# Kernel tuning notes

Hardware: AMD Instinct MI355X
Metric: run time of the kernel (lower is better)

Reference implementation:

```python
import jax, jax.numpy as jnp
import numpy as np

D = 256      # model dim
H = 8        # heads
DH = 32      # dim per head
M = 110      # nb random features = int(32*ln(32))
DEPTH = 6
DFF = 1024   # ff_mult * D


def _layer_norm(x, g, b):
    mu = jnp.mean(x, -1, keepdims=True)
    var = jnp.mean(jnp.square(x - mu), -1, keepdims=True)
    return (x - mu) * jax.lax.rsqrt(var + 1e-5) * g + b


def _softmax_kernel(x, proj, is_query):
    # FAVOR+ positive softmax kernel features (performer-pytorch softmax_kernel)
    dn = x.shape[-1] ** -0.25
    ratio = proj.shape[0] ** -0.5
    xd = jnp.einsum('bhnd,md->bhnm', x * dn, proj)
    diag = 0.5 * jnp.sum(jnp.square(x), -1, keepdims=True) * dn * dn
    stab = jnp.max(xd, -1, keepdims=True) if is_query else jnp.max(xd)
    return ratio * (jnp.exp(xd - diag - stab) + 1e-3)


def _linear_attention(q, k, v):
    # non-causal linear attention: O(N*m*d) instead of O(N^2)
    k_sum = jnp.sum(k, axis=2)                               # [B,H,m]
    d_inv = 1.0 / jnp.einsum('bhnm,bhm->bhn', q, k_sum)      # [B,H,N]
    ctx = jnp.einsum('bhnm,bhnd->bhmd', k, v)                # [B,H,m,dh]
    return jnp.einsum('bhnm,bhmd,bhn->bhnd', q, ctx, d_inv)


def _forward(expr, token_emb, cls_token, ln1_g, ln1_b, Wq, bq, Wk, bk, Wv, bv,
             Wo, bo, ln2_g, ln2_b, W1, b1, W2, b2, proj_mat, Wp, bp, top_k_genes):
    B = expr.shape[0]
    vals, _ = jax.lax.top_k(expr, top_k_genes)               # [B, k] sorted desc (matches torch.topk)
    # preprocess: L1 normalize (eps=1e-12 like F.normalize) -> *1e4 -> log1p -> 7 bins
    norm = vals / jnp.maximum(jnp.sum(jnp.abs(vals), -1, keepdims=True), 1e-12)
    e = jnp.log1p(norm * 10000.0)
    bins = jnp.linspace(0.0, jnp.max(e), 8)
    # torch.bucketize(right=False) == searchsorted side='left'
    tokens = jnp.clip(jnp.searchsorted(bins[:-1], e, side='left'), 0, 6)
    x = jnp.concatenate([jnp.broadcast_to(cls_token, (B, 1, D)), token_emb[tokens]], axis=1)
    N = x.shape[1]
    for i in range(DEPTH):
        # pre-norm FAVOR+ attention block
        h = _layer_norm(x, ln1_g[i], ln1_b[i])
        q = (h @ Wq[i] + bq[i]).reshape(B, N, H, DH).transpose(0, 2, 1, 3)
        k = (h @ Wk[i] + bk[i]).reshape(B, N, H, DH).transpose(0, 2, 1, 3)
        v = (h @ Wv[i] + bv[i]).reshape(B, N, H, DH).transpose(0, 2, 1, 3)
        qp = _softmax_kernel(q, proj_mat[i], True)
        kp = _softmax_kernel(k, proj_mat[i], False)
        o = _linear_attention(qp, kp, v).transpose(0, 2, 1, 3).reshape(B, N, D)
        x = x + o @ Wo[i] + bo[i]
        # pre-norm FFN block (GELU exact, like torch default)
        h2 = _layer_norm(x, ln2_g[i], ln2_b[i])
        x = x + jax.nn.gelu(h2 @ W1[i] + b1[i], approximate=False) @ W2[i] + b2[i]
    return x[:, 0] @ Wp + bp


def setup_inputs() -> dict:
    key = jax.random.key(0)
    ks = jax.random.split(key, 12)
    s = 0.02
    return {
        'expr': jax.random.uniform(ks[0], (8, 16906), dtype=jnp.float32),
        'token_emb': jax.random.normal(ks[1], (7, D), dtype=jnp.float32) * s,
        'cls_token': jax.random.normal(ks[2], (1, 1, D), dtype=jnp.float32),
        'ln1_g': jnp.ones((DEPTH, D), jnp.float32),
        'ln1_b': jnp.zeros((DEPTH, D), jnp.float32),
        'Wq': jax.random.normal(ks[3], (DEPTH, D, D), dtype=jnp.float32) * s,
        'bq': jnp.zeros((DEPTH, D), jnp.float32),
        'Wk': jax.random.normal(ks[4], (DEPTH, D, D), dtype=jnp.float32) * s,
        'bk': jnp.zeros((DEPTH, D), jnp.float32),
        'Wv': jax.random.normal(ks[5], (DEPTH, D, D), dtype=jnp.float32) * s,
        'bv': jnp.zeros((DEPTH, D), jnp.float32),
        'Wo': jax.random.normal(ks[6], (DEPTH, D, D), dtype=jnp.float32) * s,
        'bo': jnp.zeros((DEPTH, D), jnp.float32),
        'ln2_g': jnp.ones((DEPTH, D), jnp.float32),
        'ln2_b': jnp.zeros((DEPTH, D), jnp.float32),
        'W1': jax.random.normal(ks[7], (DEPTH, D, DFF), dtype=jnp.float32) * s,
        'b1': jnp.zeros((DEPTH, DFF), jnp.float32),
        'W2': jax.random.normal(ks[8], (DEPTH, DFF, D), dtype=jnp.float32) * s,
        'b2': jnp.zeros((DEPTH, D), jnp.float32),
        'proj_mat': jax.random.normal(ks[9], (DEPTH, M, DH), dtype=jnp.float32),
        'Wp': jax.random.normal(ks[10], (D, D), dtype=jnp.float32) * s,
        'bp': jnp.zeros((D,), jnp.float32),
        'top_k_genes': 2048,
    }


def reference(expr, token_emb, cls_token, ln1_g, ln1_b, Wq, bq, Wk, bk, Wv, bv,
              Wo, bo, ln2_g, ln2_b, W1, b1, W2, b2, proj_mat, Wp, bp, top_k_genes):
    return _forward(expr, token_emb, cls_token, ln1_g, ln1_b, Wq, bq, Wk, bk, Wv, bv,
                    Wo, bo, ln2_g, ln2_b, W1, b1, W2, b2, proj_mat, Wp, bp, top_k_genes)
```

## Files before the change

### kernel.cpp

```cpp
#include <hip/hip_runtime.h>
#include <hip/hip_bf16.h>

#define B_    8
#define NG    16906
#define KSEL  2048
#define D_    256
#define H_    8
#define DH    32
#define M_    110
#define DEPTH_ 6
#define DFF_  1024
#define N_    2049
#define BN_   (B_*N_)
#define QS    768
#define NC    8
#define NTILES 33
#define CTXE  (M_*33)
#define CTXN2 (64*CTXE)
#define NIT_TK 17

static constexpr float DN    = 0.42044820762685725f;
static constexpr float DN2   = 0.17677669529663687f;
static constexpr float RATIO = 0.09534625892455922f;

typedef __attribute__((ext_vector_type(8))) short s8v;
typedef __attribute__((ext_vector_type(4))) float f4v;

__device__ __forceinline__ unsigned floatToOrdered(float f){
  unsigned b = __float_as_uint(f);
  return (b & 0x80000000u) ? ~b : (b | 0x80000000u);
}
__device__ __forceinline__ float orderedToFloat(unsigned u){
  unsigned b = (u & 0x80000000u) ? (u & 0x7FFFFFFFu) : ~u;
  return __uint_as_float(b);
}
__device__ __forceinline__ unsigned short f2us(float f){
  __hip_bfloat16 b = __float2bfloat16(f);
  return *reinterpret_cast<unsigned short*>(&b);
}

__global__ __launch_bounds__(1024) void topk_k(const float* __restrict__ expr,
                                               float* __restrict__ selected)
{
  __shared__ unsigned histw[16*256];
  __shared__ unsigned sPrefix;
  __shared__ int sKK;
  __shared__ unsigned cGT, cEQ;
  int b = blockIdx.x, tid = threadIdx.x;
  int wv = tid >> 6, lane = tid & 63;
  const float* row = expr + (long)b*NG;
  unsigned rb[NIT_TK];
  #pragma unroll
  for (int i = 0; i < NIT_TK; i++){
    int idx = tid + i*1024;
    rb[i] = (idx < NG) ? __float_as_uint(row[idx]) : 0u;
  }
  if (tid == 0){ sPrefix = 0u; sKK = KSEL; }
  for (int pass = 0; pass < 4; ++pass){
    int shift = 24 - pass*8;
    for (int i = tid; i < 16*256; i += 1024) histw[i] = 0u;
    __syncthreads();
    unsigned pref = sPrefix;
    #pragma unroll
    for (int i = 0; i < NIT_TK; i++){
      int idx = tid + i*1024;
      unsigned bits = rb[i];
      bool ok = (idx < NG) && ((pass == 0) || ((bits >> (shift + 8)) == pref));
      if (ok) atomicAdd(&histw[wv*256 + ((bits >> shift) & 255u)], 1u);
    }
    __syncthreads();
    if (tid < 256){
      unsigned s = 0;
      #pragma unroll
      for (int w = 0; w < 16; w++) s += histw[w*256 + tid];
      histw[tid] = s;
    }
    __syncthreads();
    if (tid == 0){
      int kk = sKK; unsigned cum = 0; int sel = 0;
      for (int j = 255; j >= 0; --j){
        unsigned c = histw[j];
        if (cum + c >= (unsigned)kk){ sel = j; break; }
        cum += c;
      }
      sPrefix = (pref << 8) | (unsigned)sel;
      sKK = kk - (int)cum;
    }
    __syncthreads();
  }
  unsigned T = sPrefix; int needEQ = sKK; int base = KSEL - needEQ;
  if (tid == 0){ cGT = 0u; cEQ = 0u; }
  __syncthreads();
  #pragma unroll
  for (int i = 0; i < NIT_TK; i++){
    int idx = tid + i*1024;
    bool v = (idx < NG);
    unsigned bits = rb[i];
    bool gt = v && (bits > T);
    unsigned long long mgt = __ballot(gt);
    if (mgt){
      int leader = __ffsll((long long)mgt) - 1;
      unsigned wbase = 0;
      if (lane == leader) wbase = atomicAdd(&cGT, (unsigned)__popcll(mgt));
      wbase = __shfl(wbase, leader);
      if (gt){
        int pre = __popcll(mgt & ((1ULL << lane) - 1ULL));
        selected[(long)b*KSEL + wbase + pre] = __uint_as_float(bits);
      }
    }
    bool eq = v && (bits == T);
    unsigned long long meq = __ballot(eq);
    if (meq){
      int leader = __ffsll((long long)meq) - 1;
      unsigned wbase = 0;
      if (lane == leader) wbase = atomicAdd(&cEQ, (unsigned)__popcll(meq));
      wbase = __shfl(wbase, leader);
      if (eq){
        int pos = (int)wbase + __popcll(meq & ((1ULL << lane) - 1ULL));
        if (pos < needEQ) selected[(long)b*KSEL + base + pos] = __uint_as_float(bits);
      }
    }
  }
}

__global__ __launch_bounds__(256) void nsum_k(const float* __restrict__ selected,
                                              float* __restrict__ bsum, float* __restrict__ bv0)
{
  __shared__ float rs[256], rm[256];
  int b = blockIdx.x, tid = threadIdx.x;
  float s = 0.f, m = -INFINITY;
  for (int i = tid; i < KSEL; i += 256){ float v = selected[(long)b*KSEL + i]; s += v; m = fmaxf(m, v); }
  rs[tid] = s; rm[tid] = m; __syncthreads();
  for (int k = 128; k > 0; k >>= 1){
    if (tid < k){ rs[tid] += rs[tid + k]; rm[tid] = fmaxf(rm[tid], rm[tid + k]); }
    __syncthreads();
  }
  if (tid == 0){ bsum[b] = rs[0]; bv0[b] = rm[0]; }
}

__global__ __launch_bounds__(64) void emax_k(const float* __restrict__ bsum,
                                             const float* __restrict__ bv0,
                                             float* __restrict__ emaxp)
{
  int tid = threadIdx.x;
  float e = -INFINITY;
  if (tid < B_) e = log1pf(bv0[tid] / fmaxf(bsum[tid], 1e-12f) * 10000.0f);
  #pragma unroll
  for (int m = 1; m < 64; m <<= 1) e = fmaxf(e, __shfl_xor(e, m));
  if (tid == 0) emaxp[0] = e;
}

__global__ __launch_bounds__(64) void embed_k(const float* __restrict__ selected,
    const float* __restrict__ bsum, const float* __restrict__ emaxp,
    const float* __restrict__ temb, const float* __restrict__ cls,
    float* __restrict__ x)
{
  int rowi = blockIdx.x;
  int b = rowi / N_, n = rowi % N_;
  int tid = threadIdx.x;
  const float* src;
  if (n == 0){
    src = cls;
  } else {
    float val = selected[(long)b*KSEL + (n - 1)];
    float e = log1pf(val / fmaxf(bsum[b], 1e-12f) * 10000.0f);
    float step = emaxp[0] / 7.0f;
    int cnt = 0;
    #pragma unroll
    for (int i = 0; i < 7; i++) cnt += (((float)i * step) < e) ? 1 : 0;
    int tok = cnt > 6 ? 6 : cnt;
    src = temb + (long)tok * D_;
  }
  float4 o = *(const float4*)(src + tid*4);
  *(float4*)(x + (long)rowi*D_ + tid*4) = o;
}

__global__ __launch_bounds__(256) void ln_k(const float* __restrict__ x,
    unsigned short* __restrict__ out,
    const float* __restrict__ g, const float* __restrict__ bb)
{
  int row = blockIdx.x*4 + (threadIdx.x >> 6);
  int lane = threadIdx.x & 63;
  float4 v = *(const float4*)(x + (long)row*D_ + lane*4);
  float s = v.x + v.y + v.z + v.w;
  float q = v.x*v.x + v.y*v.y + v.z*v.z + v.w*v.w;
  #pragma unroll
  for (int m = 1; m < 64; m <<= 1){ s += __shfl_xor(s, m); q += __shfl_xor(q, m); }
  float mu  = s * (1.0f/D_);
  float var = q * (1.0f/D_) - mu*mu;
  float inv = 1.0f / sqrtf(fmaxf(var, 0.f) + 1e-5f);
  float4 gu = *(const float4*)(g + lane*4);
  float4 bu = *(const float4*)(bb + lane*4);
  ushort4 o;
  o.x = f2us((v.x - mu)*inv*gu.x + bu.x);
  o.y = f2us((v.y - mu)*inv*gu.y + bu.y);
  o.z = f2us((v.z - mu)*inv*gu.z + bu.z);
  o.w = f2us((v.w - mu)*inv*gu.w + bu.w);
  *(ushort4*)(out + (long)row*D_ + lane*4) = o;
}

__global__ __launch_bounds__(256) void wcvt_k(const float* __restrict__ src, long srcL,
    unsigned short* __restrict__ dst, long dstL, int K, int N)
{
  __shared__ float t[32][33];
  int n0 = blockIdx.x*32, k0 = blockIdx.y*32, L = blockIdx.z;
  int tx = threadIdx.x & 31, ty = threadIdx.x >> 5;
  const float* s = src + (long)L*srcL;
  for (int i = ty; i < 32; i += 8)
    t[i][tx] = s[(long)(k0+i)*N + n0 + tx];
  __syncthreads();
  unsigned short* d = dst + (long)L*dstL;
  for (int i = ty; i < 32; i += 8)
    d[(long)(n0 + i)*K + k0 + tx] = f2us(t[tx][i]);
}

__global__ __launch_bounds__(256) void pcvt_k(const float* __restrict__ proj,
                                              unsigned short* __restrict__ projb,
                                              unsigned* __restrict__ kmaxb)
{
  int L = blockIdx.x;
  if (blockIdx.x == 0 && threadIdx.x < DEPTH_) kmaxb[threadIdx.x] = 0u;
  for (int i = threadIdx.x; i < 112*32; i += 256){
    int m = i >> 5, d = i & 31;
    float v = (m < M_) ? proj[(long)L*M_*DH + m*DH + d] : 0.f;
    projb[(long)L*112*32 + i] = f2us(v);
  }
}

__global__ __launch_bounds__(256) void bcat_k(const float* __restrict__ bq,
    const float* __restrict__ bk, const float* __restrict__ bv,
    float* __restrict__ bqkv)
{
  int L = blockIdx.x;
  for (int i = threadIdx.x; i < QS; i += 256){
    float v = (i < 256) ? bq[L*256 + i] : (i < 512) ? bk[L*256 + i - 256] : bv[L*256 + i - 512];
    bqkv[(long)L*QS + i] = v;
  }
}

template<int ACT, int RES, int OUTBF>
__global__ __launch_bounds__(256) void bgemm_k(
    const unsigned short* __restrict__ A, long lda,
    const unsigned short* __restrict__ Bt,
    const float* __restrict__ bias,
    const float* __restrict__ res,
    float* __restrict__ Cf, unsigned short* __restrict__ Cb,
    int M, int Nn, int K)
{
  __shared__ __attribute__((aligned(16))) unsigned short smem[OUTBF ? 128*132 : 2*128*40];
  unsigned short* As = smem;
  unsigned short* Bs = smem + 128*40;
  int tid = threadIdx.x;
  int colBlk = blockIdx.x*128, rowBlk = blockIdx.y*128;
  int w = tid >> 6, lane = tid & 63;
  int wrow = (w >> 1)*64, wcol = (w & 1)*64;
  int fr = lane & 15, fk = (lane >> 4)*8, fq = lane >> 4;
  int srh = tid >> 2, sk8 = (tid & 3)*8;

  f4v acc[4][4];
  #pragma unroll
  for (int r = 0; r < 4; r++)
    #pragma unroll
    for (int c = 0; c < 4; c++) acc[r][c] = (f4v){0.f, 0.f, 0.f, 0.f};

  s8v pa[2], pb[2];
  #pragma unroll
  for (int half = 0; half < 2; half++){
    int r = half*64 + srh;
    int ar = rowBlk + r;
    pa[half] = (ar < M) ? *(const s8v*)(A + (long)ar*lda + sk8) : (s8v){0,0,0,0,0,0,0,0};
    pb[half] = *(const s8v*)(Bt + (long)(colBlk + r)*K + sk8);
  }

  for (int kt = 0; kt < K; kt += 32){
    __syncthreads();
    #pragma unroll
    for (int half = 0; half < 2; half++){
      int r = half*64 + srh;
      *(s8v*)&As[r*40 + sk8] = pa[half];
      *(s8v*)&Bs[r*40 + sk8] = pb[half];
    }
    __syncthreads();
    if (kt + 32 < K){
      int kn = kt + 32;
      #pragma unroll
      for (int half = 0; half < 2; half++){
        int r = half*64 + srh;
        int ar = rowBlk + r;
        pa[half] = (ar < M) ? *(const s8v*)(A + (long)ar*lda + kn + sk8) : (s8v){0,0,0,0,0,0,0,0};
        pb[half] = *(const s8v*)(Bt + (long)(colBlk + r)*K + kn + sk8);
      }
    }
    s8v a[4], b[4];
    #pragma unroll
    for (int r = 0; r < 4; r++) a[r] = *(s8v*)&As[(wrow + r*16 + fr)*40 + fk];
    #pragma unroll
    for (int c = 0; c < 4; c++) b[c] = *(s8v*)&Bs[(wcol + c*16 + fr)*40 + fk];
    #pragma unroll
    for (int r = 0; r < 4; r++)
      #pragma unroll
      for (int c = 0; c < 4; c++)
        acc[r][c] = __builtin_amdgcn_mfma_f32_16x16x32_bf16(a[r], b[c], acc[r][c], 0, 0, 0);
  }

  if (OUTBF){
    __syncthreads();
    unsigned short* Cs = smem;
    #pragma unroll
    for (int c = 0; c < 4; c++){
      int col = wcol + c*16 + fr;
      float bz = bias[colBlk + col];
      #pragma unroll
      for (int r = 0; r < 4; r++){
        #pragma unroll
        for (int j = 0; j < 4; j++){
          int rrow = wrow + r*16 + fq*4 + j;
          float val = acc[r][c][j] + bz;
          if (ACT == 1) val = 0.5f * val * (1.0f + erff(val * 0.70710678118654752f));
          Cs[rrow*132 + col] = f2us(val);
        }
      }
    }
    __syncthreads();
    for (int ci = tid; ci < 128*16; ci += 256){
      int rrow = ci >> 4, ch = ci & 15;
      int grow = rowBlk + rrow;
      if (grow < M)
        *(s8v*)(Cb + (long)grow*Nn + colBlk + ch*8) = *(s8v*)&Cs[rrow*132 + ch*8];
    }
  } else {
    #pragma unroll
    for (int c = 0; c < 4; c++){
      int col = colBlk + wcol + c*16 + fr;
      float bz = bias[col];
      #pragma unroll
      for (int r = 0; r < 4; r++){
        #pragma unroll
        for (int j = 0; j < 4; j++){
          int row = rowBlk + wrow + r*16 + fq*4 + j;
          if (row < M){
            float val = acc[r][c][j] + bz;
            if (ACT == 1) val = 0.5f * val * (1.0f + erff(val * 0.70710678118654752f));
            if (RES) val += res[(long)row*Nn + col];
            Cf[(long)row*Nn + col] = val;
          }
        }
      }
    }
  }
}

__global__ __launch_bounds__(256) void gemm_k(
    const float* __restrict__ A, long lda,
    const float* __restrict__ Bw, long ldb,
    const float* __restrict__ bias,
    float* __restrict__ Cf,
    int M, int Nn, int K)
{
  __shared__ float As[16][64];
  __shared__ float Bs[16][64];
  int tid = threadIdx.x;
  int tx = tid & 15, ty = tid >> 4;
  int rowBlk = blockIdx.x * 64, colBlk = blockIdx.y * 64;
  int am = tid >> 2, ak = (tid & 3) * 4;
  int bk = tid >> 4, bc = (tid & 15) * 4;
  float acc[4][4];
  #pragma unroll
  for (int i = 0; i < 4; i++)
    #pragma unroll
    for (int j = 0; j < 4; j++) acc[i][j] = 0.f;

  for (int kt = 0; kt < K; kt += 16){
    float4 av = make_float4(0.f, 0.f, 0.f, 0.f);
    int ar = rowBlk + am;
    if (ar < M) av = *(const float4*)(A + (long)ar*lda + kt + ak);
    As[ak+0][am] = av.x; As[ak+1][am] = av.y; As[ak+2][am] = av.z; As[ak+3][am] = av.w;
    float4 bv4 = *(const float4*)(Bw + (long)(kt + bk)*ldb + colBlk + bc);
    Bs[bk][bc+0] = bv4.x; Bs[bk][bc+1] = bv4.y;
    Bs[bk][bc+2] = bv4.z; Bs[bk][bc+3] = bv4.w;
    __syncthreads();
    #pragma unroll
    for (int kk = 0; kk < 16; kk++){
      float4 a4 = *(const float4*)&As[kk][ty*4];
      float4 b4 = *(const float4*)&Bs[kk][tx*4];
      acc[0][0] += a4.x*b4.x; acc[0][1] += a4.x*b4.y; acc[0][2] += a4.x*b4.z; acc[0][3] += a4.x*b4.w;
      acc[1][0] += a4.y*b4.x; acc[1][1] += a4.y*b4.y; acc[1][2] += a4.y*b4.z; acc[1][3] += a4.y*b4.w;
      acc[2][0] += a4.z*b4.x; acc[2][1] += a4.z*b4.y; acc[2][2] += a4.z*b4.z; acc[2][3] += a4.z*b4.w;
      acc[3][0] += a4.w*b4.x; acc[3][1] += a4.w*b4.y; acc[3][2] += a4.w*b4.z; acc[3][3] += a4.w*b4.w;
    }
    __syncthreads();
  }
  int r0 = rowBlk + ty*4, c0 = colBlk + tx*4;
  float bz[4];
  #pragma unroll
  for (int j = 0; j < 4; j++) bz[j] = bias[c0 + j];
  #pragma unroll
  for (int i = 0; i < 4; i++){
    int r = r0 + i;
    if (r < M){
      #pragma unroll
      for (int j = 0; j < 4; j++)
        Cf[(long)r*Nn + c0 + j] = acc[i][j] + bz[j];
    }
  }
}

__global__ __launch_bounds__(256) void kmax2_k(const float* __restrict__ qkv,
    const unsigned short* __restrict__ projb, unsigned* __restrict__ kmaxb)
{
  __shared__ __attribute__((aligned(16))) unsigned short ks[64*40];
  __shared__ float red[4];
  int t = blockIdx.x, h = blockIdx.y, b = blockIdx.z;
  int tid = threadIdx.x, w = tid >> 6, lane = tid & 63;
  int fr = lane & 15, fq = lane >> 4, fk = fq*8;
  int n0 = t*64;
  #pragma unroll
  for (int it = 0; it < 2; it++){
    int tok = it*32 + (tid >> 3), d4 = tid & 7;
    int n = n0 + tok;
    bool vld = (n < N_);
    long gb = ((long)(b*N_ + (vld ? n : 0)))*QS + 256 + h*DH + d4*4;
    float4 kv = vld ? *(const float4*)(qkv + gb) : make_float4(0,0,0,0);
    ushort4 ku; ku.x=f2us(kv.x); ku.y=f2us(kv.y); ku.z=f2us(kv.z); ku.w=f2us(kv.w);
    *(ushort4*)&ks[tok*40 + d4*4] = ku;
  }
  __syncthreads();
  s8v bk_ = *(s8v*)&ks[(w*16 + fr)*40 + fk];
  float mx = -INFINITY;
  int n_ = w*16 + fr;
  bool nv = (n0 + n_ < N_);
  #pragma unroll
  for (int mt = 0; mt < 7; mt++){
    s8v ap = *(const s8v*)(projb + (mt*16 + fr)*32 + fk);
    f4v z = (f4v){0.f,0.f,0.f,0.f};
    f4v xd = __builtin_amdgcn_mfma_f32_16x16x32_bf16(ap, bk_, z, 0, 0, 0);
    #pragma unroll
    for (int j = 0; j < 4; j++){
      int m = mt*16 + fq*4 + j;
      float v = (nv && m < M_) ? xd[j]*DN : -INFINITY;
      mx = fmaxf(mx, v);
    }
  }
  #pragma unroll
  for (int mk = 1; mk < 64; mk <<= 1) mx = fmaxf(mx, __shfl_xor(mx, mk));
  if (lane == 0) red[w] = mx;
  __syncthreads();
  if (tid == 0){
    float g = fmaxf(fmaxf(red[0], red[1]), fmaxf(red[2], red[3]));
    atomicMax(kmaxb, floatToOrdered(g));
  }
}

__global__ __launch_bounds__(256) void fctx_k(const float* __restrict__ qkv,
    const unsigned short* __restrict__ projb,
    const unsigned* __restrict__ kmaxb, float* __restrict__ partials)
{
  __shared__ __attribute__((aligned(16))) unsigned short ks[64*40];
  __shared__ __attribute__((aligned(16))) unsigned short vt[48*72];
  __shared__ __attribute__((aligned(16))) unsigned short kps[112*72];
  __shared__ float diags[64];
  int c = blockIdx.x, h = blockIdx.y, b = blockIdx.z;
  int tid = threadIdx.x, w = tid >> 6, lane = tid & 63;
  int fr = lane & 15, fq = lane >> 4, fk = fq*8;
  float kmax = orderedToFloat(kmaxb[0]);

  for (int i = tid; i < 15*72; i += 256) vt[33*72 + i] = 0;
  if (tid < 64) vt[32*72 + tid] = f2us(1.0f);

  s8v ap[7];
  #pragma unroll
  for (int mt = 0; mt < 7; mt++)
    ap[mt] = *(const s8v*)(projb + (mt*16 + fr)*32 + fk);

  int mt0 = w, mt1 = w + 4;
  f4v acc0[3], acc1[3];
  #pragma unroll
  for (int dt = 0; dt < 3; dt++){ acc0[dt] = (f4v){0.f,0.f,0.f,0.f}; acc1[dt] = (f4v){0.f,0.f,0.f,0.f}; }

  for (int t = c; t < NTILES; t += NC){
    int n0 = t*64;
    __syncthreads();
    #pragma unroll
    for (int it = 0; it < 2; it++){
      int tok = it*32 + (tid >> 3), d4 = tid & 7;
      int n = n0 + tok;
      bool vld = (n < N_);
      long gb = ((long)(b*N_ + (vld ? n : 0)))*QS + 256 + h*DH + d4*4;
      float4 kv = vld ? *(const float4*)(qkv + gb) : make_float4(0,0,0,0);
      float4 vv = vld ? *(const float4*)(qkv + gb + 256) : make_float4(0,0,0,0);
      ushort4 ku; ku.x=f2us(kv.x); ku.y=f2us(kv.y); ku.z=f2us(kv.z); ku.w=f2us(kv.w);
      *(ushort4*)&ks[tok*40 + d4*4] = ku;
      vt[(d4*4+0)*72 + tok] = f2us(vv.x);
      vt[(d4*4+1)*72 + tok] = f2us(vv.y);
      vt[(d4*4+2)*72 + tok] = f2us(vv.z);
      vt[(d4*4+3)*72 + tok] = f2us(vv.w);
      float sq = kv.x*kv.x + kv.y*kv.y + kv.z*kv.z + kv.w*kv.w;
      sq += __shfl_xor(sq, 1); sq += __shfl_xor(sq, 2); sq += __shfl_xor(sq, 4);
      if (d4 == 0) diags[tok] = 0.5f * DN2 * sq;
    }
    __syncthreads();
    s8v bk_ = *(s8v*)&ks[(w*16 + fr)*40 + fk];
    int n_ = w*16 + fr;
    bool nv = (n0 + n_ < N_);
    float dgn = diags[n_];
    #pragma unroll
    for (int mt = 0; mt < 7; mt++){
      f4v z = (f4v){0.f,0.f,0.f,0.f};
      f4v xd = __builtin_amdgcn_mfma_f32_16x16x32_bf16(ap[mt], bk_, z, 0, 0, 0);
      #pragma unroll
      for (int j = 0; j < 4; j++){
        float kp = nv ? RATIO*(expf(xd[j]*DN - dgn - kmax) + 1e-3f) : 0.f;
        kps[(mt*16 + fq*4 + j)*72 + n_] = f2us(kp);
      }
    }
    __syncthreads();
    #pragma unroll
    for (int kst = 0; kst < 2; kst++){
      int ko = kst*32 + fk;
      s8v b0 = *(s8v*)&vt[( 0 + fr)*72 + ko];
      s8v b1 = *(s8v*)&vt[(16 + fr)*72 + ko];
      s8v b2 = *(s8v*)&vt[(32 + fr)*72 + ko];
      s8v a0 = *(s8v*)&kps[(mt0*16 + fr)*72 + ko];
      acc0[0] = __builtin_amdgcn_mfma_f32_16x16x32_bf16(a0, b0, acc0[0], 0, 0, 0);
      acc0[1] = __builtin_amdgcn_mfma_f32_16x16x32_bf16(a0, b1, acc0[1], 0, 0, 0);
      acc0[2] = __builtin_amdgcn_mfma_f32_16x16x32_bf16(a0, b2, acc0[2], 0, 0, 0);
      if (mt1 < 7){
        s8v a1 = *(s8v*)&kps[(mt1*16 + fr)*72 + ko];
        acc1[0] = __builtin_amdgcn_mfma_f32_16x16x32_bf16(a1, b0, acc1[0], 0, 0, 0);
        acc1[1] = __builtin_amdgcn_mfma_f32_16x16x32_bf16(a1, b1, acc1[1], 0, 0, 0);
        acc1[2] = __builtin_amdgcn_mfma_f32_16x16x32_bf16(a1, b2, acc1[2], 0, 0, 0);
      }
    }
  }
  long pb = ((long)c*64 + (b*H_ + h))*CTXE;
  #pragma unroll
  for (int dt = 0; dt < 3; dt++){
    int d = dt*16 + fr;
    if (d < 33){
      #pragma unroll
      for (int j = 0; j < 4; j++){
        int m0 = mt0*16 + fq*4 + j;
        if (m0 < M_) partials[pb + m0*33 + d] = acc0[dt][j];
        if (mt1 < 7){
          int m1 = mt1*16 + fq*4 + j;
          if (m1 < M_) partials[pb + m1*33 + d] = acc1[dt][j];
        }
      }
    }
  }
}

__global__ __launch_bounds__(256) void ctxred2_k(const float* __restrict__ partials,
                                                 float* __restrict__ ctxf)
{
  int i = blockIdx.x*256 + threadIdx.x;
  if (i >= CTXN2) return;
  float s = 0.f;
  #pragma unroll
  for (int c = 0; c < NC; c++) s += partials[(long)c*CTXN2 + i];
  ctxf[i] = s;
}

__global__ __launch_bounds__(256) void attn3_k(const float* __restrict__ qkv,
    const float* __restrict__ ctxf, const unsigned short* __restrict__ projb,
    unsigned short* __restrict__ ob)
{
  __shared__ __attribute__((aligned(16))) unsigned short qs[64*40];
  __shared__ __attribute__((aligned(16))) unsigned short qps[64*136];
  __shared__ __attribute__((aligned(16))) unsigned short cst[48*136];
  __shared__ float diags[64];
  __shared__ float dens[64];
  int t = blockIdx.x, h = blockIdx.y, b = blockIdx.z;
  int tid = threadIdx.x, w = tid >> 6, lane = tid & 63;
  int fr = lane & 15, fq = lane >> 4, fk = fq*8;
  int n0 = t*64;
  long cbase = ((long)(b*H_ + h))*CTXE;

  for (int i = tid; i < 64*16; i += 256)
    qps[(i >> 4)*136 + 112 + (i & 15)] = 0;

  #pragma unroll
  for (int it = 0; it < 2; it++){
    int tok = it*32 + (tid >> 3), d4 = tid & 7;
    int n = n0 + tok;
    bool vld = (n < N_);
    long gb = ((long)(b*N_ + (vld ? n : 0)))*QS + h*DH + d4*4;
    float4 qv = vld ? *(const float4*)(qkv + gb) : make_float4(0,0,0,0);
    ushort4 qu; qu.x=f2us(qv.x); qu.y=f2us(qv.y); qu.z=f2us(qv.z); qu.w=f2us(qv.w);
    *(ushort4*)&qs[tok*40 + d4*4] = qu;
    float sq = qv.x*qv.x + qv.y*qv.y + qv.z*qv.z + qv.w*qv.w;
    sq += __shfl_xor(sq, 1); sq += __shfl_xor(sq, 2); sq += __shfl_xor(sq, 4);
    if (d4 == 0) diags[tok] = 0.5f * DN2 * sq;
  }
  for (int i = tid; i < 48*128; i += 256){
    int d = i >> 7, m = i & 127;
    float v = (d < 33 && m < M_) ? ctxf[cbase + (long)m*33 + d] : 0.f;
    cst[d*136 + m] = f2us(v);
  }
  __syncthreads();

  s8v bq_ = *(s8v*)&qs[(w*16 + fr)*40 + fk];
  int n_ = w*16 + fr;
  bool nv = (n0 + n_ < N_);
  float dgn = diags[n_];
  f4v xdv[7];
  #pragma unroll
  for (int mt = 0; mt < 7; mt++){
    s8v ap = *(const s8v*)(projb + (mt*16 + fr)*32 + fk);
    f4v z = (f4v){0.f,0.f,0.f,0.f};
    xdv[mt] = __builtin_amdgcn_mfma_f32_16x16x32_bf16(ap, bq_, z, 0, 0, 0);
  }
  float mx = -INFINITY;
  #pragma unroll
  for (int mt = 0; mt < 7; mt++)
    #pragma unroll
    for (int j = 0; j < 4; j++){
      int m = mt*16 + fq*4 + j;
      if (m < M_) mx = fmaxf(mx, xdv[mt][j]*DN);
    }
  mx = fmaxf(mx, __shfl_xor(mx, 16));
  mx = fmaxf(mx, __shfl_xor(mx, 32));
  #pragma unroll
  for (int mt = 0; mt < 7; mt++)
    #pragma unroll
    for (int j = 0; j < 4; j++){
      int m = mt*16 + fq*4 + j;
      float qp = (nv && m < M_) ? RATIO*(expf(xdv[mt][j]*DN - dgn - mx) + 1e-3f) : 0.f;
      qps[n_*136 + m] = f2us(qp);
    }
  __syncthreads();

  f4v acc[3];
  acc[0] = (f4v){0,0,0,0}; acc[1] = (f4v){0,0,0,0}; acc[2] = (f4v){0,0,0,0};
  #pragma unroll
  for (int ks = 0; ks < 4; ks++){
    int ko = ks*32 + fk;
    s8v bqp = *(s8v*)&qps[(w*16 + fr)*136 + ko];
    #pragma unroll
    for (int dt = 0; dt < 3; dt++){
      s8v ac = *(s8v*)&cst[(dt*16 + fr)*136 + ko];
      acc[dt] = __builtin_amdgcn_mfma_f32_16x16x32_bf16(ac, bqp, acc[dt], 0, 0, 0);
    }
  }
  if (fq == 0) dens[n_] = acc[2][0];
  __syncthreads();
  float dinv = 1.0f / dens[n_];
  if (nv){
    long obase = ((long)(b*N_ + n0 + n_))*D_ + h*DH;
    #pragma unroll
    for (int dt = 0; dt < 2; dt++){
      ushort4 wv;
      wv.x = f2us(acc[dt][0]*dinv);
      wv.y = f2us(acc[dt][1]*dinv);
      wv.z = f2us(acc[dt][2]*dinv);
      wv.w = f2us(acc[dt][3]*dinv);
      *(ushort4*)(ob + obase + dt*16 + fq*4) = wv;
    }
  }
}

extern "C" void kernel_launch(void* const* d_in, const int* in_sizes, int n_in,
                              void* d_out, int out_size, void* d_ws, size_t ws_size,
                              hipStream_t stream)
{
  const float* expr = (const float*)d_in[0];
  const float* temb = (const float*)d_in[1];
  const float* cls  = (const float*)d_in[2];
  const float* ln1g = (const float*)d_in[3];
  const float* ln1b = (const float*)d_in[4];
  const float* Wq   = (const float*)d_in[5];
  const float* bq   = (const float*)d_in[6];
  const float* Wk   = (const float*)d_in[7];
  const float* bk   = (const float*)d_in[8];
  const float* Wv   = (const float*)d_in[9];
  const float* bv   = (const float*)d_in[10];
  const float* Wo   = (const float*)d_in[11];
  const float* bo   = (const float*)d_in[12];
  const float* ln2g = (const float*)d_in[13];
  const float* ln2b = (const float*)d_in[14];
  const float* W1   = (const float*)d_in[15];
  const float* b1   = (const float*)d_in[16];
  const float* W2   = (const float*)d_in[17];
  const float* b2   = (const float*)d_in[18];
  const float* proj = (const float*)d_in[19];
  const float* Wp   = (const float*)d_in[20];
  const float* bp   = (const float*)d_in[21];
  (void)in_sizes; (void)n_in; (void)out_size; (void)ws_size;

  char* w = (char*)d_ws;
  size_t off = 0;
  auto alloc = [&](size_t bytes) -> char* {
    char* p = w + off;
    off = (off + bytes + 255) & ~(size_t)255;
    return p;
  };
  float*    selected = (float*)alloc((size_t)B_*KSEL*4);
  float*    bsum     = (float*)alloc(B_*4);
  float*    bv0      = (float*)alloc(B_*4);
  float*    emaxp    = (float*)alloc(4);
  unsigned* kmaxb    = (unsigned*)alloc(DEPTH_*4);
  float*    ctxf     = (float*)alloc((size_t)CTXN2*4);
  float*          x  = (float*)alloc((size_t)BN_*D_*4);
  unsigned short* h  = (unsigned short*)alloc((size_t)BN_*D_*2);
  float*        qkv  = (float*)alloc((size_t)BN_*QS*4);
  unsigned short* Wqkvt = (unsigned short*)alloc((size_t)DEPTH_*QS*D_*2);
  unsigned short* Wot = (unsigned short*)alloc((size_t)DEPTH_*D_*D_*2);
  unsigned short* W1t = (unsigned short*)alloc((size_t)DEPTH_*D_*DFF_*2);
  unsigned short* W2t = (unsigned short*)alloc((size_t)DEPTH_*DFF_*D_*2);
  unsigned short* projb = (unsigned short*)alloc((size_t)DEPTH_*112*32*2);
  float*    bqkv     = (float*)alloc((size_t)DEPTH_*QS*4);
  unsigned short* ffi = (unsigned short*)qkv;
  float*     partials = (float*)h;

  wcvt_k<<<dim3(8, 8, DEPTH_),  256, 0, stream>>>(Wq, (long)D_*D_, Wqkvt + 0,      (long)QS*D_, D_, D_);
  wcvt_k<<<dim3(8, 8, DEPTH_),  256, 0, stream>>>(Wk, (long)D_*D_, Wqkvt + 256*D_, (long)QS*D_, D_, D_);
  wcvt_k<<<dim3(8, 8, DEPTH_),  256, 0, stream>>>(Wv, (long)D_*D_, Wqkvt + 512*D_, (long)QS*D_, D_, D_);
  wcvt_k<<<dim3(8, 8, DEPTH_),  256, 0, stream>>>(Wo, (long)D_*D_,   Wot, (long)D_*D_,   D_, D_);
  wcvt_k<<<dim3(32, 8, DEPTH_), 256, 0, stream>>>(W1, (long)D_*DFF_, W1t, (long)D_*DFF_, D_, DFF_);
  wcvt_k<<<dim3(8, 32, DEPTH_), 256, 0, stream>>>(W2, (long)DFF_*D_, W2t, (long)DFF_*D_, DFF_, D_);
  pcvt_k<<<DEPTH_, 256, 0, stream>>>(proj, projb, kmaxb);
  bcat_k<<<DEPTH_, 256, 0, stream>>>(bq, bk, bv, bqkv);

  topk_k<<<B_, 1024, 0, stream>>>(expr, selected);
  nsum_k<<<B_, 256, 0, stream>>>(selected, bsum, bv0);
  emax_k<<<1, 64, 0, stream>>>(bsum, bv0, emaxp);
  embed_k<<<BN_, 64, 0, stream>>>(selected, bsum, emaxp, temb, cls, x);

  for (int L = 0; L < DEPTH_; L++){
    const unsigned short* pjb = projb + (size_t)L*112*32;
    ln_k<<<BN_/4, 256, 0, stream>>>(x, h, ln1g + L*D_, ln1b + L*D_);
    bgemm_k<0,0,0><<<dim3(6,129), 256, 0, stream>>>(h, D_, Wqkvt + (size_t)L*QS*D_, bqkv + (size_t)L*QS, nullptr, qkv, nullptr, BN_, QS, D_);
    kmax2_k<<<dim3(NTILES, H_, B_), 256, 0, stream>>>(qkv, pjb, kmaxb + L);
    fctx_k<<<dim3(NC, H_, B_), 256, 0, stream>>>(qkv, pjb, kmaxb + L, partials);
    ctxred2_k<<<(CTXN2 + 255)/256, 256, 0, stream>>>(partials, ctxf);
    attn3_k<<<dim3(NTILES, H_, B_), 256, 0, stream>>>(qkv, ctxf, pjb, h);
    bgemm_k<0,1,0><<<dim3(2,129), 256, 0, stream>>>(h, D_, Wot + (size_t)L*D_*D_, bo + L*D_, x, x, nullptr, BN_, D_, D_);
    ln_k<<<BN_/4, 256, 0, stream>>>(x, h, ln2g + L*D_, ln2b + L*D_);
    bgemm_k<1,0,1><<<dim3(8,129), 256, 0, stream>>>(h, D_, W1t + (size_t)L*D_*DFF_, b1 + L*DFF_, nullptr, nullptr, ffi, BN_, DFF_, D_);
    bgemm_k<0,1,0><<<dim3(2,129), 256, 0, stream>>>(ffi, DFF_, W2t + (size_t)L*DFF_*D_, b2 + L*D_, x, x, nullptr, BN_, D_, DFF_);
  }
  gemm_k<<<dim3(1,4), 256, 0, stream>>>(x, (long)N_*D_, Wp, D_, bp,
                                        (float*)d_out, B_, D_, D_);
}
```

Measured before the change: 1.426 ms.

## Parallelize radix-select bin search and double-buffer GEMM shared tiles

```diff
diff --git a/kernel.cpp b/kernel.cpp
--- a/kernel.cpp
+++ b/kernel.cpp
@@ -61,6 +61,7 @@
     for (int i = tid; i < 16*256; i += 1024) histw[i] = 0u;
     __syncthreads();
     unsigned pref = sPrefix;
+    unsigned kk  = (unsigned)sKK;
     #pragma unroll
     for (int i = 0; i < NIT_TK; i++){
       int idx = tid + i*1024;
@@ -76,15 +77,21 @@
       histw[tid] = s;
     }
     __syncthreads();
-    if (tid == 0){
-      int kk = sKK; unsigned cum = 0; int sel = 0;
-      for (int j = 255; j >= 0; --j){
-        unsigned c = histw[j];
-        if (cum + c >= (unsigned)kk){ sel = j; break; }
-        cum += c;
-      }
-      sPrefix = (pref << 8) | (unsigned)sel;
-      sKK = kk - (int)cum;
+    unsigned* bufA = histw;
+    unsigned* bufB = histw + 256;
+    for (int d = 1; d < 256; d <<= 1){
+      if (tid < 256)
+        bufB[tid] = bufA[tid] + ((tid + d < 256) ? bufA[tid + d] : 0u);
+      __syncthreads();
+      unsigned* t = bufA; bufA = bufB; bufB = t;
+    }
+    if (tid < 256){
+      unsigned sj  = bufA[tid];
+      unsigned sj1 = (tid < 255) ? bufA[tid + 1] : 0u;
+      if (sj >= kk && sj1 < kk){
+        sPrefix = (pref << 8) | (unsigned)tid;
+        sKK = (int)(kk - sj1);
+      }
     }
     __syncthreads();
   }
@@ -247,9 +254,7 @@
     float* __restrict__ Cf, unsigned short* __restrict__ Cb,
     int M, int Nn, int K)
 {
-  __shared__ __attribute__((aligned(16))) unsigned short smem[OUTBF ? 128*132 : 2*128*40];
-  unsigned short* As = smem;
-  unsigned short* Bs = smem + 128*40;
+  __shared__ __attribute__((aligned(16))) unsigned short smem[2*2*128*40];
   int tid = threadIdx.x;
   int colBlk = blockIdx.x*128, rowBlk = blockIdx.y*128;
   int w = tid >> 6, lane = tid & 63;
@@ -272,8 +277,10 @@
     pb[half] = *(const s8v*)(Bt + (long)(colBlk + r)*K + sk8);
   }
 
-  for (int kt = 0; kt < K; kt += 32){
-    __syncthreads();
+  int it = 0;
+  for (int kt = 0; kt < K; kt += 32, ++it){
+    unsigned short* As = smem + (it & 1)*(2*128*40);
+    unsigned short* Bs = As + 128*40;
     #pragma unroll
     for (int half = 0; half < 2; half++){
       int r = half*64 + srh;
```

After: 1.386 ms. 1.03x faster.
